# Optimization experiments

Hardware: AMD Instinct MI355X
Metric: run time of the kernel (lower is better)

## Reference

```python
import jax, jax.numpy as jnp
import numpy as np

N_SLOTS = 65536  # memory rows
D_FEAT = 64      # memory feature dim
BATCH = 2048


def setup_inputs() -> dict:
    key = jax.random.key(0)
    k1, k2 = jax.random.split(key)
    memory = jax.random.normal(k1, (N_SLOTS, D_FEAT), dtype=jnp.float32)
    weight = jax.random.normal(k2, (BATCH, N_SLOTS), dtype=jnp.float32)
    return {"memory": memory, "weight": weight}


def reference(memory, weight):
    # softmax over the memory-slot axis, then batched read: [B,N] @ [N,D] -> [B,D]
    w = jax.nn.softmax(weight, axis=1)
    return jnp.einsum('bn,nd->bd', w, memory)
```

## Files before the change

kernel.cpp:

```cpp
#include <hip/hip_runtime.h>
#include <hip/hip_bf16.h>
#include <stdint.h>

typedef __attribute__((ext_vector_type(8))) short short8;
typedef __attribute__((ext_vector_type(4))) float f32x4;

#define N_SLOTS 65536
#define D_FEAT  64
#define BATCH   2048
#define BM      64
#define BK      128
#define NC      32
#define NITER   16

__device__ __forceinline__ unsigned short f2bf(float f) {
    unsigned int u = __builtin_bit_cast(unsigned int, f);
    u += 0x7fffu + ((u >> 16) & 1u);
    return (unsigned short)(u >> 16);
}
__device__ __forceinline__ unsigned int pk2(float a, float b) {
    return (unsigned int)f2bf(a) | ((unsigned int)f2bf(b) << 16);
}

__global__ __launch_bounds__(256) void convert_mt(const float* __restrict__ M,
                                                  unsigned short* __restrict__ MT) {
    __shared__ unsigned short s[64][72];
    const int t  = threadIdx.x;
    const int k0 = blockIdx.x * 64;
    #pragma unroll
    for (int j = 0; j < 4; ++j) {
        const int r = j * 16 + (t >> 4);
        const int c = (t & 15) * 4;
        const float4 v = *reinterpret_cast<const float4*>(M + (size_t)(k0 + r) * D_FEAT + c);
        s[r][c + 0] = f2bf(v.x); s[r][c + 1] = f2bf(v.y);
        s[r][c + 2] = f2bf(v.z); s[r][c + 3] = f2bf(v.w);
    }
    __syncthreads();
    #pragma unroll
    for (int j = 0; j < 2; ++j) {
        const int d  = j * 32 + (t >> 3);
        const int kk = (t & 7) * 8;
        short8 v;
        #pragma unroll
        for (int e = 0; e < 8; ++e) v[e] = (short)s[kk + e][d];
        *reinterpret_cast<short8*>(MT + (size_t)d * N_SLOTS + k0 + kk) = v;
    }
}

__global__ __launch_bounds__(256) void reading_main(
    const unsigned short* __restrict__ MT,
    const float* __restrict__ W,
    float* __restrict__ out,
    float* __restrict__ lrow)
{
    __shared__ __align__(16) unsigned short sA[BM * BK];
    __shared__ __align__(16) unsigned short sB[D_FEAT * BK];

    const int t  = threadIdx.x;
    const int ln = t & 63;
    const int wv = t >> 6;
    const int r  = ln & 15;
    const int g  = ln >> 4;
    const int hi = ln >> 5;

    const int bid = blockIdx.x;
    const int wg  = ((bid & 7) << 7) | (bid >> 3);
    const int by  = wg >> 5;
    const int bx  = wg & 31;
    const int bm0 = bx * BM;

    const int    kq    = (ln & 31) * 4;
    const size_t wbase = (size_t)(bm0 + wv * 16 + hi) * N_SLOTS + kq;
    const int    sd    = wv * 16 + (ln >> 4);
    const int    kb    = (ln & 15) * 8;
    const size_t mbase = (size_t)sd * N_SLOTS + kb;

    #define COLOF(s) ((size_t)(((((s) + bx) & (NITER - 1)) * NC + by) * BK))

    float lsum[8];
    #pragma unroll
    for (int j = 0; j < 8; ++j) lsum[j] = 0.f;
    f32x4 acc[4];
    #pragma unroll
    for (int td = 0; td < 4; ++td) acc[td] = f32x4{0.f, 0.f, 0.f, 0.f};

    f32x4  pw[8];
    short8 pm[4];

    #define ISSUE(co) do { \
        _Pragma("unroll") for (int j = 0; j < 8; ++j) \
            pw[j] = __builtin_nontemporal_load( \
                reinterpret_cast<const f32x4*>(W + wbase + (size_t)j * 2 * N_SLOTS + (co))); \
        _Pragma("unroll") for (int i = 0; i < 4; ++i) \
            pm[i] = *reinterpret_cast<const short8*>(MT + mbase + (size_t)i * 4 * N_SLOTS + (co)); \
    } while (0)

    #define WRITE_STAGE() do { \
        _Pragma("unroll") for (int j = 0; j < 8; ++j) { \
            const float e0 = __expf(pw[j][0]), e1 = __expf(pw[j][1]); \
            const float e2 = __expf(pw[j][2]), e3 = __expf(pw[j][3]); \
            lsum[j] += (e0 + e1) + (e2 + e3); \
            const unsigned long long pk = (unsigned long long)pk2(e0, e1) \
                                        | ((unsigned long long)pk2(e2, e3) << 32); \
            const int rj = wv * 16 + j * 2 + hi; \
            *reinterpret_cast<unsigned long long*>(&sA[rj * BK + (kq ^ ((rj & 7) * 8))]) = pk; \
        } \
        _Pragma("unroll") for (int i = 0; i < 4; ++i) { \
            const int d = sd + i * 4; \
            *reinterpret_cast<short8*>(&sB[d * BK + (kb ^ ((d & 7) * 8))]) = pm[i]; \
        } \
    } while (0)

    #define COMPUTE() do { \
        _Pragma("unroll") for (int ks = 0; ks < 4; ++ks) { \
            const int ko = (ks * 32 + g * 8) ^ ((r & 7) * 8); \
            const short8 a = *reinterpret_cast<const short8*>(&sA[(16 * wv + r) * BK + ko]); \
            _Pragma("unroll") for (int td = 0; td < 4; ++td) { \
                const short8 b = *reinterpret_cast<const short8*>(&sB[(16 * td + r) * BK + ko]); \
                acc[td] = __builtin_amdgcn_mfma_f32_16x16x32_bf16(a, b, acc[td], 0, 0, 0); \
            } \
        } \
    } while (0)

    #define BAR_PLAIN() do { \
        __builtin_amdgcn_sched_barrier(0); \
        __builtin_amdgcn_s_barrier(); \
        __builtin_amdgcn_sched_barrier(0); \
    } while (0)

    #define BAR_LGKM() do { \
        __builtin_amdgcn_sched_barrier(0); \
        asm volatile("s_waitcnt lgkmcnt(0)" ::: "memory"); \
        __builtin_amdgcn_s_barrier(); \
        __builtin_amdgcn_sched_barrier(0); \
    } while (0)

    ISSUE(COLOF(0));
    WRITE_STAGE();
    BAR_LGKM();

    #pragma unroll 1
    for (int s = 0; s < NITER; ++s) {
        const bool more = (s + 1 < NITER);
        if (more) { ISSUE(COLOF(s + 1)); __builtin_amdgcn_sched_barrier(0); }
        COMPUTE();
        if (more) {
            BAR_PLAIN();
            WRITE_STAGE();
            BAR_LGKM();
        }
    }

    #pragma unroll
    for (int td = 0; td < 4; ++td) {
        #pragma unroll
        for (int q = 0; q < 4; ++q) {
            atomicAdd(&out[(size_t)(bm0 + 16 * wv + g * 4 + q) * D_FEAT + 16 * td + r],
                      acc[td][q]);
        }
    }

    #pragma unroll
    for (int j = 0; j < 8; ++j) {
        float s2 = lsum[j];
        s2 += __shfl_xor(s2, 1, 64);
        s2 += __shfl_xor(s2, 2, 64);
        s2 += __shfl_xor(s2, 4, 64);
        s2 += __shfl_xor(s2, 8, 64);
        s2 += __shfl_xor(s2, 16, 64);
        if ((ln & 31) == 0)
            atomicAdd(&lrow[bm0 + wv * 16 + j * 2 + hi], s2);
    }
}

__global__ __launch_bounds__(256) void reading_finalize(
    float* __restrict__ out, const float* __restrict__ lrow)
{
    const int i = blockIdx.x * 256 + threadIdx.x;
    out[i] = out[i] / lrow[i >> 6];
}

extern "C" void kernel_launch(void* const* d_in, const int* in_sizes, int n_in,
                              void* d_out, int out_size, void* d_ws, size_t ws_size,
                              hipStream_t stream) {
    const float* M = (const float*)d_in[0];
    const float* W = (const float*)d_in[1];
    float* out = (float*)d_out;

    float*          lrow = (float*)d_ws;
    unsigned short* MT   = (unsigned short*)((char*)d_ws + (1 << 16));

    hipMemsetAsync(d_out, 0, (size_t)BATCH * D_FEAT * sizeof(float), stream);
    hipMemsetAsync(d_ws, 0, (size_t)BATCH * sizeof(float), stream);

    convert_mt<<<N_SLOTS / 64, 256, 0, stream>>>(M, MT);
    reading_main<<<(BATCH / BM) * NC, 256, 0, stream>>>(MT, W, out, lrow);
    reading_finalize<<<(BATCH * D_FEAT) / 256, 256, 0, stream>>>(out, lrow);
}
```

Measured before the change: 117.6 us.

## Double-buffer weight register prefetch two stages ahead in main loop

```diff
diff --git a/kernel.cpp b/kernel.cpp
--- a/kernel.cpp
+++ b/kernel.cpp
@@ -47,7 +47,7 @@
     }
 }
 
-__global__ __launch_bounds__(256) void reading_main(
+__global__ __launch_bounds__(256, 3) void reading_main(
     const unsigned short* __restrict__ MT,
     const float* __restrict__ W,
     float* __restrict__ out,
@@ -84,21 +84,24 @@
     #pragma unroll
     for (int td = 0; td < 4; ++td) acc[td] = f32x4{0.f, 0.f, 0.f, 0.f};
 
-    f32x4  pw[8];
+    f32x4  pwA[8], pwB[8];
     short8 pm[4];
 
-    #define ISSUE(co) do { \
+    #define ISSUE_W(buf, co) do { \
         _Pragma("unroll") for (int j = 0; j < 8; ++j) \
-            pw[j] = __builtin_nontemporal_load( \
+            buf[j] = __builtin_nontemporal_load( \
                 reinterpret_cast<const f32x4*>(W + wbase + (size_t)j * 2 * N_SLOTS + (co))); \
+    } while (0)
+
+    #define ISSUE_M(co) do { \
         _Pragma("unroll") for (int i = 0; i < 4; ++i) \
             pm[i] = *reinterpret_cast<const short8*>(MT + mbase + (size_t)i * 4 * N_SLOTS + (co)); \
     } while (0)
 
-    #define WRITE_STAGE() do { \
+    #define WRITE_STAGE(buf) do { \
         _Pragma("unroll") for (int j = 0; j < 8; ++j) { \
-            const float e0 = __expf(pw[j][0]), e1 = __expf(pw[j][1]); \
-            const float e2 = __expf(pw[j][2]), e3 = __expf(pw[j][3]); \
+            const float e0 = __expf(buf[j][0]), e1 = __expf(buf[j][1]); \
+            const float e2 = __expf(buf[j][2]), e3 = __expf(buf[j][3]); \
             lsum[j] += (e0 + e1) + (e2 + e3); \
             const unsigned long long pk = (unsigned long long)pk2(e0, e1) \
                                         | ((unsigned long long)pk2(e2, e3) << 32); \
@@ -135,18 +138,31 @@
         __builtin_amdgcn_sched_barrier(0); \
     } while (0)
 
-    ISSUE(COLOF(0));
-    WRITE_STAGE();
+    ISSUE_M(COLOF(0));
+    ISSUE_W(pwA, COLOF(0));
+    ISSUE_W(pwB, COLOF(1));
+    WRITE_STAGE(pwA);
     BAR_LGKM();
 
     #pragma unroll 1
-    for (int s = 0; s < NITER; ++s) {
-        const bool more = (s + 1 < NITER);
-        if (more) { ISSUE(COLOF(s + 1)); __builtin_amdgcn_sched_barrier(0); }
+    for (int s = 0; s < NITER; s += 2) {
+        ISSUE_M(COLOF(s + 1));
+        if (s + 2 < NITER) ISSUE_W(pwA, COLOF(s + 2));
+        __builtin_amdgcn_sched_barrier(0);
         COMPUTE();
-        if (more) {
+        BAR_PLAIN();
+        WRITE_STAGE(pwB);
+        BAR_LGKM();
+
+        if (s + 2 < NITER) {
+            ISSUE_M(COLOF(s + 2));
+            if (s + 3 < NITER) ISSUE_W(pwB, COLOF(s + 3));
+            __builtin_amdgcn_sched_barrier(0);
+        }
+        COMPUTE();
+        if (s + 2 < NITER) {
             BAR_PLAIN();
-            WRITE_STAGE();
+            WRITE_STAGE(pwA);
             BAR_LGKM();
         }
     }
```

New measurement: 116.6 us. About the same (-0.8%).
